# Performance work log

Hardware: AMD Instinct MI355X
Metric: run time of the kernel (lower is better)

## Reference

```python
import jax, jax.numpy as jnp
import numpy as np

B, N, C, H, W = 16, 10, 128, 48, 48

def setup_inputs() -> dict:
    key = jax.random.key(0)
    k0, k1 = jax.random.split(key, 2)
    x = jax.random.normal(k0, (B, N, C, H, W), dtype=jnp.float32)
    # trainable interpolation params, initialized to 0.5 as in the torch module
    pos_dec = jnp.full((N,), 0.5, dtype=jnp.float32)
    length_dec = jnp.full((N,), 0.5, dtype=jnp.float32)
    # 1x1 conv == channel-mixing matmul over N*C channels
    NC = N * C
    conv_w = jax.random.normal(k1, (NC, NC), dtype=jnp.float32) * (1.0 / np.sqrt(NC))
    conv_b = jnp.zeros((NC,), dtype=jnp.float32)
    return {"x": x, "pos_dec": pos_dec, "length_dec": length_dec,
            "conv_w": conv_w, "conv_b": conv_b}


def reference(x, pos_dec, length_dec, conv_w, conv_b):
    b, n, c, h, w = x.shape
    d = c * h * w
    q = x.reshape(b, n, d)          # proj_query (B,N,CHW)
    k = q                           # proj_key has the same flattened features
    # bi_interpolate with pos_int=i, length_int=1 reduces in closed form to:
    #   s0 = (1-pd)*K[i]   + pd*K[i+1]                      (key_short row)
    #   s1 = ld*((1-pd)*K[i+1] + pd*K[i+2])                 (zero-padded short mixed with key_long)
    # where indices wrap mod N (key was concatenated with itself).
    idx = jnp.arange(n)
    k1_ = k[:, (idx + 1) % n]       # (B,N,D)
    k2_ = k[:, (idx + 2) % n]
    pd = pos_dec[None, :, None]
    ld = length_dec[None, :, None]
    s0 = (1.0 - pd) * k + pd * k1_
    s1 = ld * ((1.0 - pd) * k1_ + pd * k2_)
    S = jnp.stack([s0, s1], axis=2)                 # (B,N,2,D) interpolated keys per group
    logits = jnp.einsum('bnd,bnkd->bnk', q, S)      # per-group 2-way attention scores
    attn = jax.nn.softmax(logits, axis=-1)          # softmax over the 2 searched keys
    out = jnp.einsum('bnk,bnkd->bnd', attn, S)      # (B,N,D)
    feat = out.reshape(b, n * c, h, w)
    conv = jnp.einsum('oc,bchw->bohw', conv_w, feat) + conv_b[None, :, None, None]
    return conv + x.reshape(b, n * c, h, w)
```

## Files before the change

### kernel.cpp

```cpp
#include <hip/hip_runtime.h>
#include <hip/hip_bf16.h>

#define BB 16
#define NN 10
#define CC 128
#define HWD 2304
#define DD (CC*HWD)
#define NC (NN*CC)
#define CHK 36
#define CHUNK (DD/CHK)

#define BM 256
#define BN 256
#define BK 64
#define TK (NC/BK)

typedef __bf16 bf16x8 __attribute__((ext_vector_type(8)));
typedef float  f32x4  __attribute__((ext_vector_type(4)));

#define FEAT_BYTES ((size_t)BB*HWD*NC*2)
#define WB_BYTES   ((size_t)NC*NC*2)
#define PART_FLOATS (BB*NN*CHK*3)

__device__ __forceinline__ ushort f2bf(float f) {
    __hip_bfloat16 h = __float2bfloat16(f);
    return *reinterpret_cast<ushort*>(&h);
}

__device__ __forceinline__ void gload_lds16(const ushort* g, ushort* l) {
    __builtin_amdgcn_global_load_lds(
        (const __attribute__((address_space(1))) void*)(const void*)g,
        (__attribute__((address_space(3))) void*)(void*)l,
        16, 0, 0);
}

__global__ __launch_bounds__(256) void k_dots(const float* __restrict__ x,
                                              float* __restrict__ part) {
    int blk = blockIdx.x;
    int bn = blk / CHK, ch = blk % CHK;
    int b = bn / NN, n = bn % NN;
    int n1 = (n + 1) % NN, n2 = (n + 2) % NN;
    const float* p0 = x + ((size_t)b*NN + n )*DD + (size_t)ch*CHUNK;
    const float* p1 = x + ((size_t)b*NN + n1)*DD + (size_t)ch*CHUNK;
    const float* p2 = x + ((size_t)b*NN + n2)*DD + (size_t)ch*CHUNK;
    int t = threadIdx.x;
    float s0 = 0.f, s1 = 0.f, s2 = 0.f;
    #pragma unroll
    for (int i = 0; i < CHUNK/1024; ++i) {
        int off = i*1024 + t*4;
        float4 a = *(const float4*)(p0 + off);
        float4 u = *(const float4*)(p1 + off);
        float4 v = *(const float4*)(p2 + off);
        s0 += a.x*a.x + a.y*a.y + a.z*a.z + a.w*a.w;
        s1 += a.x*u.x + a.y*u.y + a.z*u.z + a.w*u.w;
        s2 += a.x*v.x + a.y*v.y + a.z*v.z + a.w*v.w;
    }
    for (int o = 32; o > 0; o >>= 1) {
        s0 += __shfl_down(s0, o);
        s1 += __shfl_down(s1, o);
        s2 += __shfl_down(s2, o);
    }
    __shared__ float red[4][3];
    int w = t >> 6, l = t & 63;
    if (l == 0) { red[w][0] = s0; red[w][1] = s1; red[w][2] = s2; }
    __syncthreads();
    if (t == 0) {
        float r0 = 0.f, r1 = 0.f, r2 = 0.f;
        for (int i = 0; i < 4; ++i) { r0 += red[i][0]; r1 += red[i][1]; r2 += red[i][2]; }
        float* o = part + ((size_t)bn*CHK + ch)*3;
        o[0] = r0; o[1] = r1; o[2] = r2;
    }
}

__global__ void k_coef(const float* __restrict__ part,
                       const float* __restrict__ pos_dec,
                       const float* __restrict__ len_dec,
                       float* __restrict__ coef) {
    int bn = threadIdx.x;
    if (bn >= BB*NN) return;
    int n = bn % NN;
    float d0 = 0.f, d1 = 0.f, d2 = 0.f;
    const float* p = part + (size_t)bn*CHK*3;
    for (int i = 0; i < CHK; ++i) { d0 += p[i*3]; d1 += p[i*3+1]; d2 += p[i*3+2]; }
    float pd = pos_dec[n], ld = len_dec[n];
    float l0 = (1.f - pd)*d0 + pd*d1;
    float l1 = ld*((1.f - pd)*d1 + pd*d2);
    float m  = fmaxf(l0, l1);
    float e0 = expf(l0 - m), e1 = expf(l1 - m);
    float inv = 1.f/(e0 + e1);
    float a0 = e0*inv, a1 = e1*inv;
    coef[bn*3+0] = a0*(1.f - pd);
    coef[bn*3+1] = a0*pd + a1*ld*(1.f - pd);
    coef[bn*3+2] = a1*ld*pd;
}

__global__ __launch_bounds__(256) void k_wconv(const float* __restrict__ w,
                                               ushort* __restrict__ wb) {
    int i = blockIdx.x*blockDim.x + threadIdx.x;
    size_t idx = (size_t)i*4;
    if (idx >= (size_t)NC*NC) return;
    float4 a = *(const float4*)(w + idx);
    ushort4 o;
    o.x = f2bf(a.x); o.y = f2bf(a.y); o.z = f2bf(a.z); o.w = f2bf(a.w);
    *(ushort4*)(wb + idx) = o;
}

__global__ __launch_bounds__(256) void k_feat(const float* __restrict__ x,
                                              const float* __restrict__ coef,
                                              ushort* __restrict__ featT) {
    __shared__ float tile[32*129];
    int hwt = blockIdx.x;
    int n   = blockIdx.y;
    int b   = blockIdx.z;
    int bn  = b*NN + n;
    float c0 = coef[bn*3+0], c1 = coef[bn*3+1], c2 = coef[bn*3+2];
    int n1 = (n + 1) % NN, n2 = (n + 2) % NN;
    const float* p0 = x + ((size_t)b*NN + n )*DD;
    const float* p1 = x + ((size_t)b*NN + n1)*DD;
    const float* p2 = x + ((size_t)b*NN + n2)*DD;
    int t = threadIdx.x;
    int hw0 = hwt*32;

    int ccl = t >> 3;
    int hwi = (t & 7) * 4;
    #pragma unroll
    for (int p = 0; p < 4; ++p) {
        int cc = p*32 + ccl;
        size_t off = (size_t)cc*HWD + hw0 + hwi;
        float4 a = *(const float4*)(p0 + off);
        float4 u = *(const float4*)(p1 + off);
        float4 v = *(const float4*)(p2 + off);
        tile[(hwi+0)*129 + cc] = c0*a.x + c1*u.x + c2*v.x;
        tile[(hwi+1)*129 + cc] = c0*a.y + c1*u.y + c2*v.y;
        tile[(hwi+2)*129 + cc] = c0*a.z + c1*u.z + c2*v.z;
        tile[(hwi+3)*129 + cc] = c0*a.w + c1*u.w + c2*v.w;
    }
    __syncthreads();

    int hwl = t >> 4;
    int cc0 = (t & 15) * 8;
    #pragma unroll
    for (int p = 0; p < 2; ++p) {
        int hw = p*16 + hwl;
        const float* src = &tile[hw*129 + cc0];
        union { ushort us[8]; uint4 v; } pk;
        #pragma unroll
        for (int j = 0; j < 8; ++j) pk.us[j] = f2bf(src[j]);
        ushort* dst = featT + (size_t)b*HWD*NC + (size_t)(hw0 + hw)*NC + n*CC + cc0;
        *(uint4*)dst = pk.v;
    }
}

__device__ __forceinline__ void stage_tile(const ushort* __restrict__ Ag,
                                           const ushort* __restrict__ Bg,
                                           ushort* as, ushort* bs,
                                           int t, int kO) {
    int r  = t >> 3;
    int kc = ((t & 7) ^ (r & 7)) * 8;
    #pragma unroll
    for (int p = 0; p < 4; ++p)
        gload_lds16(Ag + (size_t)(p*64 + r)*NC + kO + kc, as + p*4096 + t*8);
    #pragma unroll
    for (int p = 0; p < 4; ++p)
        gload_lds16(Bg + (size_t)(p*64 + r)*NC + kO + kc, bs + p*4096 + t*8);
}

__global__ __launch_bounds__(512, 2) void k_gemm(const ushort* __restrict__ Wb,
                                                 const ushort* __restrict__ featT,
                                                 const float* __restrict__ bias,
                                                 const float* __restrict__ x,
                                                 float* __restrict__ out) {
    __shared__ ushort As[2][BM*BK];
    __shared__ ushort Bs[2][BN*BK];

    int bid = blockIdx.x;
    int wkid = (bid & 7) * 90 + (bid >> 3);
    int b   = wkid / 45;
    int r45 = wkid % 45;
    int hwt = r45 / 5;
    int ot  = r45 % 5;
    int o0 = ot*BM, hw0 = hwt*BN;

    int t = threadIdx.x;
    int l = t & 63;
    int w = t >> 6;
    int wr = w >> 2, wc = w & 3;

    const ushort* Ag = Wb + (size_t)o0*NC;
    const ushort* Bg = featT + (size_t)b*HWD*NC + (size_t)hw0*NC;

    int rowA = wr*128 + (l & 15);
    int rowB = wc*64  + (l & 15);
    int cA   = l >> 4;
    int xr   = l & 7;

    f32x4 acc[8][4] = {};

    stage_tile(Ag, Bg, As[0], Bs[0], t, 0);
    stage_tile(Ag, Bg, As[1], Bs[1], t, BK);
    asm volatile("s_waitcnt vmcnt(8)" ::: "memory");
    __builtin_amdgcn_s_barrier();
    __builtin_amdgcn_sched_barrier(0);

    for (int kt = 0; kt < TK; ++kt) {
        int cur = kt & 1;
        const ushort* as = As[cur];
        const ushort* bs = Bs[cur];

        #pragma unroll
        for (int kq = 0; kq < 2; ++kq) {
            bf16x8 bfr[4];
            #pragma unroll
            for (int n = 0; n < 4; ++n)
                bfr[n] = *(const bf16x8*)&bs[(rowB + n*16)*BK + ((((kq<<2)|cA) ^ xr)<<3)];
            #pragma unroll
            for (int mq = 0; mq < 2; ++mq) {
                bf16x8 afr[4];
                #pragma unroll
                for (int i = 0; i < 4; ++i)
                    afr[i] = *(const bf16x8*)&as[(rowA + mq*64 + i*16)*BK + ((((kq<<2)|cA) ^ xr)<<3)];
                __builtin_amdgcn_s_setprio(1);
                #pragma unroll
                for (int i = 0; i < 4; ++i)
                    #pragma unroll
                    for (int n = 0; n < 4; ++n)
                        acc[mq*4+i][n] = __builtin_amdgcn_mfma_f32_16x16x32_bf16(
                            afr[i], bfr[n], acc[mq*4+i][n], 0, 0, 0);
                __builtin_amdgcn_s_setprio(0);
            }
        }

        asm volatile("" ::: "memory");
        __builtin_amdgcn_s_barrier();
        __builtin_amdgcn_sched_barrier(0);

        if (kt + 2 < TK) {
            stage_tile(Ag, Bg, As[cur], Bs[cur], t, (kt+2)*BK);
            asm volatile("s_waitcnt vmcnt(8)" ::: "memory");
        } else {
            asm volatile("s_waitcnt vmcnt(0)" ::: "memory");
        }
        __builtin_amdgcn_s_barrier();
        __builtin_amdgcn_sched_barrier(0);
    }

    #pragma unroll
    for (int m = 0; m < 8; ++m) {
        int ro_base = o0 + wr*128 + m*16 + ((l >> 4) << 2);
        #pragma unroll
        for (int n = 0; n < 4; ++n) {
            int col = hw0 + wc*64 + n*16 + (l & 15);
            #pragma unroll
            for (int r = 0; r < 4; ++r) {
                int ro = ro_base + r;
                size_t idx = (size_t)b*NC*HWD + (size_t)ro*HWD + col;
                out[idx] = acc[m][n][r] + bias[ro] + x[idx];
            }
        }
    }
}

extern "C" void kernel_launch(void* const* d_in, const int* in_sizes, int n_in,
                              void* d_out, int out_size, void* d_ws, size_t ws_size,
                              hipStream_t stream) {
    const float* x       = (const float*)d_in[0];
    const float* pos_dec = (const float*)d_in[1];
    const float* len_dec = (const float*)d_in[2];
    const float* conv_w  = (const float*)d_in[3];
    const float* conv_b  = (const float*)d_in[4];
    float* out = (float*)d_out;

    char* ws = (char*)d_ws;
    ushort* featT = (ushort*)ws;
    ushort* wb    = (ushort*)(ws + FEAT_BYTES);
    float*  part  = (float*)(ws + FEAT_BYTES + WB_BYTES);
    float*  coef  = part + PART_FLOATS;

    k_dots <<<dim3(BB*NN*CHK), 256, 0, stream>>>(x, part);
    k_coef <<<dim3(1), 256, 0, stream>>>(part, pos_dec, len_dec, coef);
    k_wconv<<<dim3(1600), 256, 0, stream>>>(conv_w, wb);
    k_feat <<<dim3(72, NN, BB), 256, 0, stream>>>(x, coef, featT);
    k_gemm <<<dim3(720), 512, 0, stream>>>(wb, featT, conv_b, x, out);
}
```

Measured before the change: 322.4 us.

## Restructure GEMM main loop into 4-stage BK=32 pipeline with interleaved staging

```diff
diff --git a/kernel.cpp b/kernel.cpp
--- a/kernel.cpp
+++ b/kernel.cpp
@@ -12,8 +12,8 @@
 
 #define BM 256
 #define BN 256
-#define BK 64
-#define TK (NC/BK)
+#define BK2 32
+#define NHALF (NC/BK2)
 
 typedef __bf16 bf16x8 __attribute__((ext_vector_type(8)));
 typedef float  f32x4  __attribute__((ext_vector_type(4)));
@@ -151,27 +151,12 @@
     }
 }
 
-__device__ __forceinline__ void stage_tile(const ushort* __restrict__ Ag,
-                                           const ushort* __restrict__ Bg,
-                                           ushort* as, ushort* bs,
-                                           int t, int kO) {
-    int r  = t >> 3;
-    int kc = ((t & 7) ^ (r & 7)) * 8;
-    #pragma unroll
-    for (int p = 0; p < 4; ++p)
-        gload_lds16(Ag + (size_t)(p*64 + r)*NC + kO + kc, as + p*4096 + t*8);
-    #pragma unroll
-    for (int p = 0; p < 4; ++p)
-        gload_lds16(Bg + (size_t)(p*64 + r)*NC + kO + kc, bs + p*4096 + t*8);
-}
-
 __global__ __launch_bounds__(512, 2) void k_gemm(const ushort* __restrict__ Wb,
                                                  const ushort* __restrict__ featT,
                                                  const float* __restrict__ bias,
                                                  const float* __restrict__ x,
                                                  float* __restrict__ out) {
-    __shared__ ushort As[2][BM*BK];
-    __shared__ ushort Bs[2][BN*BK];
+    __shared__ ushort S[4][2][BM*BK2];
 
     int bid = blockIdx.x;
     int wkid = (bid & 7) * 90 + (bid >> 3);
@@ -189,60 +174,77 @@
     const ushort* Ag = Wb + (size_t)o0*NC;
     const ushort* Bg = featT + (size_t)b*HWD*NC + (size_t)hw0*NC;
 
-    int rowA = wr*128 + (l & 15);
-    int rowB = wc*64  + (l & 15);
-    int cA   = l >> 4;
-    int xr   = l & 7;
+    int sl0 = t, sl1 = 512 + t;
+    int sr0 = sl0 >> 2, sc0 = sl0 & 3;
+    int sr1 = sl1 >> 2, sc1 = sl1 & 3;
+    size_t ga0 = (size_t)sr0*NC + (size_t)((sc0 ^ ((sr0 >> 1) & 3)) * 8);
+    size_t ga1 = (size_t)sr1*NC + (size_t)((sc1 ^ ((sr1 >> 1) & 3)) * 8);
+
+#define STAGE_A(ht_) do { ushort* d_ = &S[(ht_)&3][0][0]; size_t ko_ = (size_t)(ht_)*BK2; \
+    gload_lds16(Ag + ga0 + ko_, d_ + sl0*8); \
+    gload_lds16(Ag + ga1 + ko_, d_ + sl1*8); } while(0)
+#define STAGE_B(ht_) do { ushort* d_ = &S[(ht_)&3][1][0]; size_t ko_ = (size_t)(ht_)*BK2; \
+    gload_lds16(Bg + ga0 + ko_, d_ + sl0*8); \
+    gload_lds16(Bg + ga1 + ko_, d_ + sl1*8); } while(0)
+
+    int rowA0 = wr*128 + (l & 15);
+    int rowB0 = wc*64  + (l & 15);
+    int ksw   = ((l >> 4) ^ ((l >> 1) & 3)) * 8;
 
     f32x4 acc[8][4] = {};
 
-    stage_tile(Ag, Bg, As[0], Bs[0], t, 0);
-    stage_tile(Ag, Bg, As[1], Bs[1], t, BK);
+    STAGE_A(0); STAGE_B(0);
+    STAGE_A(1); STAGE_B(1);
+    STAGE_A(2); STAGE_B(2);
     asm volatile("s_waitcnt vmcnt(8)" ::: "memory");
     __builtin_amdgcn_s_barrier();
     __builtin_amdgcn_sched_barrier(0);
 
-    for (int kt = 0; kt < TK; ++kt) {
-        int cur = kt & 1;
-        const ushort* as = As[cur];
-        const ushort* bs = Bs[cur];
-
-        #pragma unroll
-        for (int kq = 0; kq < 2; ++kq) {
-            bf16x8 bfr[4];
+    for (int ht = 0; ht < NHALF; ++ht) {
+        const ushort* as = &S[ht & 3][0][0];
+        const ushort* bs = &S[ht & 3][1][0];
+
+        bf16x8 bfr[4], af0[4], af1[4];
+        #pragma unroll
+        for (int n = 0; n < 4; ++n)
+            bfr[n] = *(const bf16x8*)&bs[(rowB0 + n*16)*BK2 + ksw];
+        #pragma unroll
+        for (int i = 0; i < 4; ++i)
+            af0[i] = *(const bf16x8*)&as[(rowA0 + i*16)*BK2 + ksw];
+        if (ht + 3 < NHALF) STAGE_A(ht + 3);
+        __builtin_amdgcn_s_barrier();
+        __builtin_amdgcn_sched_barrier(0);
+        __builtin_amdgcn_s_setprio(1);
+        #pragma unroll
+        for (int i = 0; i < 4; ++i)
             #pragma unroll
             for (int n = 0; n < 4; ++n)
-                bfr[n] = *(const bf16x8*)&bs[(rowB + n*16)*BK + ((((kq<<2)|cA) ^ xr)<<3)];
+                acc[i][n] = __builtin_amdgcn_mfma_f32_16x16x32_bf16(af0[i], bfr[n], acc[i][n], 0, 0, 0);
+        __builtin_amdgcn_s_setprio(0);
+        __builtin_amdgcn_s_barrier();
+        __builtin_amdgcn_sched_barrier(0);
+
+        #pragma unroll
+        for (int i = 0; i < 4; ++i)
+            af1[i] = *(const bf16x8*)&as[(rowA0 + 64 + i*16)*BK2 + ksw];
+        if (ht + 3 < NHALF) STAGE_B(ht + 3);
+        if (ht < NHALF - 3)       asm volatile("s_waitcnt vmcnt(8)" ::: "memory");
+        else if (ht == NHALF - 3) asm volatile("s_waitcnt vmcnt(4)" ::: "memory");
+        else if (ht == NHALF - 2) asm volatile("s_waitcnt vmcnt(0)" ::: "memory");
+        __builtin_amdgcn_s_barrier();
+        __builtin_amdgcn_sched_barrier(0);
+        __builtin_amdgcn_s_setprio(1);
+        #pragma unroll
+        for (int i = 0; i < 4; ++i)
             #pragma unroll
-            for (int mq = 0; mq < 2; ++mq) {
-                bf16x8 afr[4];
-                #pragma unroll
-                for (int i = 0; i < 4; ++i)
-                    afr[i] = *(const bf16x8*)&as[(rowA + mq*64 + i*16)*BK + ((((kq<<2)|cA) ^ xr)<<3)];
-                __builtin_amdgcn_s_setprio(1);
-                #pragma unroll
-                for (int i = 0; i < 4; ++i)
-                    #pragma unroll
-                    for (int n = 0; n < 4; ++n)
-                        acc[mq*4+i][n] = __builtin_amdgcn_mfma_f32_16x16x32_bf16(
-                            afr[i], bfr[n], acc[mq*4+i][n], 0, 0, 0);
-                __builtin_amdgcn_s_setprio(0);
-            }
-        }
-
-        asm volatile("" ::: "memory");
-        __builtin_amdgcn_s_barrier();
-        __builtin_amdgcn_sched_barrier(0);
-
-        if (kt + 2 < TK) {
-            stage_tile(Ag, Bg, As[cur], Bs[cur], t, (kt+2)*BK);
-            asm volatile("s_waitcnt vmcnt(8)" ::: "memory");
-        } else {
-            asm volatile("s_waitcnt vmcnt(0)" ::: "memory");
-        }
-        __builtin_amdgcn_s_barrier();
-        __builtin_amdgcn_sched_barrier(0);
-    }
+            for (int n = 0; n < 4; ++n)
+                acc[4+i][n] = __builtin_amdgcn_mfma_f32_16x16x32_bf16(af1[i], bfr[n], acc[4+i][n], 0, 0, 0);
+        __builtin_amdgcn_s_setprio(0);
+        __builtin_amdgcn_s_barrier();
+        __builtin_amdgcn_sched_barrier(0);
+    }
+#undef STAGE_A
+#undef STAGE_B
 
     #pragma unroll
     for (int m = 0; m < 8; ++m) {
```

Result: faster. 305.8 us (-5.2%).
